# Performance work log

Measured on AMD Instinct MI355X. Metric: run time of the kernel, lower is better.

The kernel has to match this reference:

```python
import jax, jax.numpy as jnp
import numpy as np

ALPHA = 0.2  # LeakyReLU negative slope


def _gat_layer(x, xq, src, dst, W_l, a_l, N):
    # x, xq: [N, Din]; W_l: [Din, D]; a_l: [2*D]
    h = x @ W_l            # [N, D]
    hq = xq @ W_l          # [N, D]
    D = W_l.shape[1]
    # a @ cat(hq[src], h[dst]) splits into two per-node dot products
    sq = hq @ a_l[:D]      # [N]
    sn = h @ a_l[D:]       # [N]
    s = sq[src] + sn[dst]  # [E]
    e = jnp.exp(-jnp.where(s >= 0, s, ALPHA * s))          # [E]
    rowsum = jax.ops.segment_sum(e, src, num_segments=N)    # [N]
    agg = jax.ops.segment_sum(e[:, None] * h[dst], src, num_segments=N)  # [N, D]
    denom = jnp.where(rowsum == 0, 1.0, rowsum)[:, None]
    h_prime = agg / denom
    # torch replaces NaN (0/0) with 0; isolated nodes -> 0
    return jnp.where(rowsum[:, None] == 0, 0.0, h_prime)


def setup_inputs() -> dict:
    key = jax.random.key(0)
    k1, k2, k3, k4, k5 = jax.random.split(key, 5)
    B, N, D, E, L = 2, 20000, 256, 320000, 2
    nodes = jax.random.normal(k1, (B, N, D), dtype=jnp.float32)
    nodes_query = jax.random.normal(k2, (B, N, D), dtype=jnp.float32)
    W = jax.random.normal(k3, (L, D, D), dtype=jnp.float32) * 0.088  # xavier_normal gain=1.414
    a = jax.random.normal(k4, (L, 2 * D), dtype=jnp.float32) * 0.074
    edges = jax.random.randint(k5, (B, 2, E), 0, N, dtype=jnp.int32)
    return {"nodes": nodes, "nodes_query": nodes_query, "W": W, "a": a, "edges": edges}


def reference(nodes, nodes_query, W, a, edges):
    B, N, D = nodes.shape
    L = W.shape[0]

    def per_graph(x, xq, e):
        src, dst = e[0], e[1]
        h = x
        for l in range(L):  # small fixed layer count
            h = _gat_layer(h, xq, src, dst, W[l], a[l], N)
        return h

    out = jax.vmap(per_graph)(nodes, nodes_query, edges)
    return out + nodes  # residual
```

## Files before the change

### kernel.cpp

```cpp
#include <hip/hip_runtime.h>
#include <hip/hip_fp16.h>
#include <math.h>

constexpr int N = 20000, D = 256, E = 320000, B = 2, L = 2;

typedef __bf16 bf16x8 __attribute__((ext_vector_type(8)));
typedef float f32x4 __attribute__((ext_vector_type(4)));

__device__ __forceinline__ unsigned short f2bf(float f) {
  unsigned int u = __float_as_uint(f);
  u = (u + 0x7FFF + ((u >> 16) & 1)) >> 16;
  return (unsigned short)u;
}
__device__ __forceinline__ unsigned short f2h(float f) {
  __half h = __float2half(f);
  return *(unsigned short*)&h;
}
__device__ __forceinline__ float2 h2f(unsigned int u) {
  __half2 hv = *reinterpret_cast<__half2*>(&u);
  return __half22float2(hv);
}

__global__ void tobf_kernel(const float* __restrict__ in, unsigned short* __restrict__ out,
                            int n8) {
  int i = blockIdx.x * blockDim.x + threadIdx.x;
  if (i < n8) {
    float4 v0 = ((const float4*)in)[i * 2];
    float4 v1 = ((const float4*)in)[i * 2 + 1];
    unsigned short t[8] = {f2bf(v0.x), f2bf(v0.y), f2bf(v0.z), f2bf(v0.w),
                           f2bf(v1.x), f2bf(v1.y), f2bf(v1.z), f2bf(v1.w)};
    ((uint4*)out)[i] = *(uint4*)t;
  }
}

__global__ void count_kernel(const int* __restrict__ edges, int* __restrict__ counts) {
  int e = blockIdx.x * blockDim.x + threadIdx.x;
  if (e < B * E) {
    int b = (e >= E) ? 1 : 0;
    int s = edges[(size_t)b * E + e];
    atomicAdd(&counts[b * N + s], 1);
  }
}

__global__ __launch_bounds__(1024) void scan_kernel(const int* __restrict__ counts,
                                                    int* __restrict__ rowstart) {
  constexpr int CHUNK = 20;
  __shared__ int sums[1024];
  int b = blockIdx.x;
  const int* c = counts + b * N;
  int* rs = rowstart + b * (N + 1);
  int tid = threadIdx.x;
  int base = tid * CHUNK;
  int local[CHUNK];
  int s = 0;
#pragma unroll
  for (int i = 0; i < CHUNK; ++i) {
    int g = base + i;
    int v = (g < N) ? c[g] : 0;
    local[i] = s;
    s += v;
  }
  sums[tid] = s;
  __syncthreads();
  for (int off = 1; off < 1024; off <<= 1) {
    int t = (tid >= off) ? sums[tid - off] : 0;
    __syncthreads();
    sums[tid] += t;
    __syncthreads();
  }
  int prev = (tid == 0) ? 0 : sums[tid - 1];
#pragma unroll
  for (int i = 0; i < CHUNK; ++i) {
    int g = base + i;
    if (g < N) rs[g] = prev + local[i];
  }
  if (tid == 1023) rs[N] = sums[1023];
}

__global__ void scatter_kernel(const int* __restrict__ edges, const int* __restrict__ rowstart,
                               int* __restrict__ fill, int* __restrict__ csr) {
  int e = blockIdx.x * blockDim.x + threadIdx.x;
  if (e < B * E) {
    int b = (e >= E) ? 1 : 0;
    int s = edges[(size_t)b * E + e];
    int d = edges[(size_t)(b + 1) * E + e];
    int p = rowstart[b * (N + 1) + s] + atomicAdd(&fill[b * N + s], 1);
    csr[(size_t)b * E + p] = d;
  }
}

__global__ void wt_kernel(const float* __restrict__ W, unsigned short* __restrict__ Wt) {
  __shared__ float t[16][17];
  int l = blockIdx.z;
  int k = blockIdx.y * 16 + threadIdx.y;
  int n = blockIdx.x * 16 + threadIdx.x;
  t[threadIdx.y][threadIdx.x] = W[l * 65536 + k * 256 + n];
  __syncthreads();
  int nn = blockIdx.x * 16 + threadIdx.y;
  int kk = blockIdx.y * 16 + threadIdx.x;
  Wt[l * 65536 + nn * 256 + kk] = f2bf(t[threadIdx.x][threadIdx.y]);
}

__global__ void wa_kernel(const float* __restrict__ W, const float* __restrict__ a,
                          float* __restrict__ wa) {
  int l = blockIdx.x;
  int k = threadIdx.x;
  float s = 0.f;
  for (int d = 0; d < D; ++d) s += W[l * 65536 + k * D + d] * a[l * 2 * D + d];
  wa[l * D + k] = s;
}

__global__ void sq_kernel(const float* __restrict__ xq, const float* __restrict__ wa,
                          float* __restrict__ sq) {
  int wave = (blockIdx.x * blockDim.x + threadIdx.x) >> 6;
  int lane = threadIdx.x & 63;
  int b = blockIdx.y;
  if (wave >= N) return;
  const float4 xv = *(const float4*)(xq + ((size_t)b * N + wave) * D + (lane << 2));
  const float4 w0 = *(const float4*)(wa + (lane << 2));
  const float4 w1 = *(const float4*)(wa + D + (lane << 2));
  float s0 = xv.x * w0.x + xv.y * w0.y + xv.z * w0.z + xv.w * w0.w;
  float s1 = xv.x * w1.x + xv.y * w1.y + xv.z * w1.z + xv.w * w1.w;
  for (int off = 32; off; off >>= 1) {
    s0 += __shfl_down(s0, off);
    s1 += __shfl_down(s1, off);
  }
  if (lane == 0) {
    sq[(b * 2 + 0) * N + wave] = s0;
    sq[(b * 2 + 1) * N + wave] = s1;
  }
}

__global__ __launch_bounds__(256) void gemm_mfma(const unsigned short* __restrict__ A,
                                                 const unsigned short* __restrict__ Wt,
                                                 unsigned short* __restrict__ Ch,
                                                 const float* __restrict__ a2,
                                                 float* __restrict__ sn, int M) {
  __shared__ unsigned short As[128 * 32];
  __shared__ unsigned short Bs[64 * 32];
  int z = blockIdx.z;
  const unsigned short* Az = A + (size_t)z * M * 256;
  unsigned short* Cz = Ch + (size_t)z * M * 256;
  float* snz = sn + (size_t)z * M;
  int tid = threadIdx.x;
  int bm = blockIdx.y * 128, bn = blockIdx.x * 64;
  int wv = tid >> 6, lane = tid & 63;
  int lm = lane & 15, lq = lane >> 4;
  f32x4 acc[2][4] = {};

  for (int k0 = 0; k0 < 256; k0 += 32) {
    int m = tid >> 1, kb = (tid & 1) << 4;
    if (bm + m < M) {
      const unsigned short* ap = Az + (size_t)(bm + m) * 256 + k0 + kb;
      *(uint4*)&As[m * 32 + kb] = *(const uint4*)ap;
      *(uint4*)&As[m * 32 + kb + 8] = *(const uint4*)(ap + 8);
    } else {
      uint4 z4 = make_uint4(0, 0, 0, 0);
      *(uint4*)&As[m * 32 + kb] = z4;
      *(uint4*)&As[m * 32 + kb + 8] = z4;
    }
    int nn = tid >> 2, kb2 = (tid & 3) << 3;
    *(uint4*)&Bs[nn * 32 + kb2] = *(const uint4*)(Wt + (size_t)(bn + nn) * 256 + k0 + kb2);
    __syncthreads();

    bf16x8 af0 = *(const bf16x8*)&As[(wv * 32 + lm) * 32 + lq * 8];
    bf16x8 af1 = *(const bf16x8*)&As[(wv * 32 + 16 + lm) * 32 + lq * 8];
#pragma unroll
    for (int nf = 0; nf < 4; ++nf) {
      bf16x8 bfr = *(const bf16x8*)&Bs[(nf * 16 + lm) * 32 + lq * 8];
      acc[0][nf] = __builtin_amdgcn_mfma_f32_16x16x32_bf16(af0, bfr, acc[0][nf], 0, 0, 0);
      acc[1][nf] = __builtin_amdgcn_mfma_f32_16x16x32_bf16(af1, bfr, acc[1][nf], 0, 0, 0);
    }
    __syncthreads();
  }

  float a2v[4];
#pragma unroll
  for (int nf = 0; nf < 4; ++nf) a2v[nf] = a2[bn + nf * 16 + lm];
#pragma unroll
  for (int f = 0; f < 2; ++f) {
#pragma unroll
    for (int r = 0; r < 4; ++r) {
      int row = bm + wv * 32 + f * 16 + lq * 4 + r;
      if (row < M) {
        float partial = 0.f;
#pragma unroll
        for (int nf = 0; nf < 4; ++nf) {
          float v = acc[f][nf][r];
          Cz[(size_t)row * 256 + bn + nf * 16 + lm] = f2h(v);
          partial += v * a2v[nf];
        }
        partial += __shfl_xor(partial, 1);
        partial += __shfl_xor(partial, 2);
        partial += __shfl_xor(partial, 4);
        partial += __shfl_xor(partial, 8);
        if (lm == 0) atomicAdd(&snz[row], partial);
      }
    }
  }
}

__global__ __launch_bounds__(256) void agg_kernel(const int* __restrict__ rowstart,
                                                  const int* __restrict__ csr,
                                                  const float* __restrict__ sq_all,
                                                  const float* __restrict__ sn,
                                                  const unsigned short* __restrict__ hhf,
                                                  const float* __restrict__ resid,
                                                  float* __restrict__ outf,
                                                  unsigned short* __restrict__ outbf, int l) {
  int b = blockIdx.y;
  int tid = threadIdx.x, wv = tid >> 6, lane = tid & 63;
  int node = blockIdx.x * 4 + wv;
  if (node >= N) return;
  int eg = lane >> 5, dl = lane & 31;
  const int* rs = rowstart + b * (N + 1);
  const int* cs = csr + (size_t)b * E;
  const float* snb = sn + (size_t)b * N;
  const unsigned short* hb = hhf + (size_t)b * N * 256;
  int beg = rs[node], end = rs[node + 1];
  float sqv = sq_all[((b << 1) + l) * N + node];
  float wsum = 0.f;
  float acc[8] = {};
  for (int c0 = beg; c0 < end; c0 += 64) {
    int cnt = min(end - c0, 64);
    int idx = 0;
    float w = 0.f;
    if (lane < cnt) {
      idx = cs[c0 + lane];
      float s = sqv + snb[idx];
      float lr = (s >= 0.f) ? s : 0.2f * s;
      w = __expf(-lr);
    }
    wsum += w;
#pragma unroll 4
    for (int j = eg; j < cnt; j += 2) {
      int dsti = __shfl(idx, j);
      float wj = __shfl(w, j);
      uint4 hv = *(const uint4*)(hb + (size_t)dsti * 256 + (dl << 3));
      float2 f0 = h2f(hv.x), f1 = h2f(hv.y), f2 = h2f(hv.z), f3 = h2f(hv.w);
      acc[0] = fmaf(wj, f0.x, acc[0]);
      acc[1] = fmaf(wj, f0.y, acc[1]);
      acc[2] = fmaf(wj, f1.x, acc[2]);
      acc[3] = fmaf(wj, f1.y, acc[3]);
      acc[4] = fmaf(wj, f2.x, acc[4]);
      acc[5] = fmaf(wj, f2.y, acc[5]);
      acc[6] = fmaf(wj, f3.x, acc[6]);
      acc[7] = fmaf(wj, f3.y, acc[7]);
    }
  }
  for (int off = 32; off; off >>= 1) wsum += __shfl_xor(wsum, off);
#pragma unroll
  for (int i = 0; i < 8; ++i) acc[i] += __shfl_xor(acc[i], 32);
  float inv = (wsum > 0.f) ? 1.f / wsum : 0.f;
  float o0 = (eg ? acc[4] : acc[0]) * inv;
  float o1 = (eg ? acc[5] : acc[1]) * inv;
  float o2 = (eg ? acc[6] : acc[2]) * inv;
  float o3 = (eg ? acc[7] : acc[3]) * inv;
  size_t rowoff = ((size_t)b * N + node) * 256 + (dl << 3) + (eg << 2);
  if (outbf) {
    unsigned short t[4] = {f2bf(o0), f2bf(o1), f2bf(o2), f2bf(o3)};
    *(uint2*)(outbf + rowoff) = *(uint2*)t;
  } else {
    const float4 rv = *(const float4*)(resid + rowoff);
    *(float4*)(outf + rowoff) = make_float4(o0 + rv.x, o1 + rv.y, o2 + rv.z, o3 + rv.w);
  }
}

extern "C" void kernel_launch(void* const* d_in, const int* in_sizes, int n_in,
                              void* d_out, int out_size, void* d_ws, size_t ws_size,
                              hipStream_t stream) {
  const float* nodes = (const float*)d_in[0];
  const float* nodesq = (const float*)d_in[1];
  const float* W = (const float*)d_in[2];
  const float* a = (const float*)d_in[3];
  const int* edges = (const int*)d_in[4];
  float* out = (float*)d_out;

  const size_t ND = (size_t)N * D;
  unsigned short* hhf = (unsigned short*)d_ws;
  unsigned short* h1bf = hhf + (size_t)B * ND;
  unsigned short* nbf = h1bf + (size_t)B * ND;
  unsigned short* Wt = nbf + (size_t)B * ND;
  float* ws_f = (float*)(Wt + (size_t)L * D * D);
  float* sn = ws_f;
  float* sq_all = sn + B * N;
  float* wa = sq_all + (size_t)B * L * N;
  int* wsi = (int*)(wa + L * D);
  int* counts = wsi;
  int* fill = counts + B * N;
  int* rowstart = fill + B * N;
  int* csr = rowstart + B * (N + 1);

  wt_kernel<<<dim3(16, 16, 2), dim3(16, 16), 0, stream>>>(W, Wt);
  wa_kernel<<<2, 256, 0, stream>>>(W, a, wa);
  int n8 = (int)(B * ND / 8);
  tobf_kernel<<<(n8 + 255) / 256, 256, 0, stream>>>(nodes, nbf, n8);

  hipMemsetAsync(counts, 0, (size_t)2 * B * N * sizeof(int), stream);
  count_kernel<<<(B * E + 255) / 256, 256, 0, stream>>>(edges, counts);
  scan_kernel<<<B, 1024, 0, stream>>>(counts, rowstart);
  scatter_kernel<<<(B * E + 255) / 256, 256, 0, stream>>>(edges, rowstart, fill, csr);

  int nwave_blocks = (N * 64 + 255) / 256;
  sq_kernel<<<dim3(nwave_blocks, B), 256, 0, stream>>>(nodesq, wa, sq_all);

  for (int l = 0; l < L; ++l) {
    const float* al2 = a + (size_t)l * 2 * D + D;
    const unsigned short* Acur = (l == 0) ? nbf : h1bf;
    hipMemsetAsync(sn, 0, (size_t)B * N * sizeof(float), stream);
    gemm_mfma<<<dim3(4, (N + 127) / 128, B), 256, 0, stream>>>(Acur, Wt + (size_t)l * D * D,
                                                               hhf, al2, sn, N);
    bool last = (l == L - 1);
    agg_kernel<<<dim3((N + 3) / 4, B), 256, 0, stream>>>(rowstart, csr, sq_all, sn, hhf,
                                                         last ? nodes : nullptr,
                                                         last ? out : nullptr,
                                                         last ? nullptr : h1bf, l);
  }
}
```

Measured before the change: 358.4 us.

## Merge preprocessing launches, drop memsets, and software-pipeline row gathers in aggregation

Several small setup kernels (weight transpose, W·a, bf16 conversion, sq projection, edge counting) and the memsets are merged into two multi-role launches. Zeroing of the sn buffers and the counts/fill arrays is folded into the prep kernel by laying them out contiguously. Each layer now gets its own sn buffer, so the per-layer memset goes away. In the aggregation kernel, neighbour feature loads are issued ahead of the exp/weight computation and double-buffered four at a time, to hide gather latency. The cost is higher register pressure in agg_kernel and more complex branching in the fused kernels.

```diff
diff --git a/kernel.cpp b/kernel.cpp
--- a/kernel.cpp
+++ b/kernel.cpp
@@ -21,21 +21,66 @@
   return __half22float2(hv);
 }
 
-__global__ void tobf_kernel(const float* __restrict__ in, unsigned short* __restrict__ out,
-                            int n8) {
-  int i = blockIdx.x * blockDim.x + threadIdx.x;
-  if (i < n8) {
-    float4 v0 = ((const float4*)in)[i * 2];
-    float4 v1 = ((const float4*)in)[i * 2 + 1];
+__global__ __launch_bounds__(256) void prep_kernel(const float* __restrict__ W,
+                                                   const float* __restrict__ a,
+                                                   unsigned short* __restrict__ Wt,
+                                                   float* __restrict__ wa,
+                                                   uint4* __restrict__ zbase) {
+  int bi = blockIdx.x, tid = threadIdx.x;
+  if (bi < 512) {
+    __shared__ float t[16][17];
+    int l = bi >> 8, rem = bi & 255;
+    int by = rem >> 4, bx = rem & 15;
+    int tx = tid & 15, ty = tid >> 4;
+    t[ty][tx] = W[l * 65536 + (by * 16 + ty) * 256 + bx * 16 + tx];
+    __syncthreads();
+    Wt[l * 65536 + (bx * 16 + ty) * 256 + by * 16 + tx] = f2bf(t[tx][ty]);
+  } else if (bi < 514) {
+    int l = bi - 512;
+    float s = 0.f;
+    for (int d = 0; d < D; ++d) s += W[l * 65536 + tid * D + d] * a[l * 2 * D + d];
+    wa[l * D + tid] = s;
+  } else {
+    int zi = (bi - 514) * 256 + tid;
+    if (zi < 40000) zbase[zi] = make_uint4(0, 0, 0, 0);
+  }
+}
+
+__global__ __launch_bounds__(256) void tsc_kernel(const float* __restrict__ nodes,
+                                                  unsigned short* __restrict__ nbf,
+                                                  const float* __restrict__ xq,
+                                                  const float* __restrict__ wa,
+                                                  float* __restrict__ sq,
+                                                  const int* __restrict__ edges,
+                                                  int* __restrict__ counts) {
+  int bi = blockIdx.x, tid = threadIdx.x;
+  if (bi < 10000) {
+    int b = (bi >= 5000) ? 1 : 0;
+    int blk = bi - b * 5000;
+    int wave = blk * 4 + (tid >> 6);
+    int lane = tid & 63;
+    const float4 xv = *(const float4*)(xq + ((size_t)b * N + wave) * D + (lane << 2));
+    const float4 w0 = *(const float4*)(wa + (lane << 2));
+    const float4 w1 = *(const float4*)(wa + D + (lane << 2));
+    float s0 = xv.x * w0.x + xv.y * w0.y + xv.z * w0.z + xv.w * w0.w;
+    float s1 = xv.x * w1.x + xv.y * w1.y + xv.z * w1.z + xv.w * w1.w;
+    for (int off = 32; off; off >>= 1) {
+      s0 += __shfl_down(s0, off);
+      s1 += __shfl_down(s1, off);
+    }
+    if (lane == 0) {
+      sq[(b * 2 + 0) * N + wave] = s0;
+      sq[(b * 2 + 1) * N + wave] = s1;
+    }
+  } else if (bi < 15000) {
+    int i = (bi - 10000) * 256 + tid;
+    float4 v0 = ((const float4*)nodes)[i * 2];
+    float4 v1 = ((const float4*)nodes)[i * 2 + 1];
     unsigned short t[8] = {f2bf(v0.x), f2bf(v0.y), f2bf(v0.z), f2bf(v0.w),
                            f2bf(v1.x), f2bf(v1.y), f2bf(v1.z), f2bf(v1.w)};
-    ((uint4*)out)[i] = *(uint4*)t;
-  }
-}
-
-__global__ void count_kernel(const int* __restrict__ edges, int* __restrict__ counts) {
-  int e = blockIdx.x * blockDim.x + threadIdx.x;
-  if (e < B * E) {
+    ((uint4*)nbf)[i] = *(uint4*)t;
+  } else {
+    int e = (bi - 15000) * 256 + tid;
     int b = (e >= E) ? 1 : 0;
     int s = edges[(size_t)b * E + e];
     atomicAdd(&counts[b * N + s], 1);
@@ -86,48 +131,6 @@
     int d = edges[(size_t)(b + 1) * E + e];
     int p = rowstart[b * (N + 1) + s] + atomicAdd(&fill[b * N + s], 1);
     csr[(size_t)b * E + p] = d;
-  }
-}
-
-__global__ void wt_kernel(const float* __restrict__ W, unsigned short* __restrict__ Wt) {
-  __shared__ float t[16][17];
-  int l = blockIdx.z;
-  int k = blockIdx.y * 16 + threadIdx.y;
-  int n = blockIdx.x * 16 + threadIdx.x;
-  t[threadIdx.y][threadIdx.x] = W[l * 65536 + k * 256 + n];
-  __syncthreads();
-  int nn = blockIdx.x * 16 + threadIdx.y;
-  int kk = blockIdx.y * 16 + threadIdx.x;
-  Wt[l * 65536 + nn * 256 + kk] = f2bf(t[threadIdx.x][threadIdx.y]);
-}
-
-__global__ void wa_kernel(const float* __restrict__ W, const float* __restrict__ a,
-                          float* __restrict__ wa) {
-  int l = blockIdx.x;
-  int k = threadIdx.x;
-  float s = 0.f;
-  for (int d = 0; d < D; ++d) s += W[l * 65536 + k * D + d] * a[l * 2 * D + d];
-  wa[l * D + k] = s;
-}
-
-__global__ void sq_kernel(const float* __restrict__ xq, const float* __restrict__ wa,
-                          float* __restrict__ sq) {
-  int wave = (blockIdx.x * blockDim.x + threadIdx.x) >> 6;
-  int lane = threadIdx.x & 63;
-  int b = blockIdx.y;
-  if (wave >= N) return;
-  const float4 xv = *(const float4*)(xq + ((size_t)b * N + wave) * D + (lane << 2));
-  const float4 w0 = *(const float4*)(wa + (lane << 2));
-  const float4 w1 = *(const float4*)(wa + D + (lane << 2));
-  float s0 = xv.x * w0.x + xv.y * w0.y + xv.z * w0.z + xv.w * w0.w;
-  float s1 = xv.x * w1.x + xv.y * w1.y + xv.z * w1.z + xv.w * w1.w;
-  for (int off = 32; off; off >>= 1) {
-    s0 += __shfl_down(s0, off);
-    s1 += __shfl_down(s1, off);
-  }
-  if (lane == 0) {
-    sq[(b * 2 + 0) * N + wave] = s0;
-    sq[(b * 2 + 1) * N + wave] = s1;
   }
 }
 
@@ -224,28 +227,50 @@
   for (int c0 = beg; c0 < end; c0 += 64) {
     int cnt = min(end - c0, 64);
     int idx = 0;
-    float w = 0.f;
+    float snv = 0.f;
     if (lane < cnt) {
       idx = cs[c0 + lane];
-      float s = sqv + snb[idx];
-      float lr = (s >= 0.f) ? s : 0.2f * s;
-      w = __expf(-lr);
-    }
+      snv = snb[idx];
+    }
+    int nj = (cnt - eg + 1) >> 1;
+    uint4 hv[4];
+#pragma unroll
+    for (int u = 0; u < 4; ++u) {
+      int dsti = __shfl(idx, eg + 2 * u);
+      if (u < nj) hv[u] = *(const uint4*)(hb + (size_t)dsti * 256 + (dl << 3));
+    }
+    float s = sqv + snv;
+    float lr = (s >= 0.f) ? s : 0.2f * s;
+    float w = (lane < cnt) ? __expf(-lr) : 0.f;
     wsum += w;
-#pragma unroll 4
-    for (int j = eg; j < cnt; j += 2) {
-      int dsti = __shfl(idx, j);
-      float wj = __shfl(w, j);
-      uint4 hv = *(const uint4*)(hb + (size_t)dsti * 256 + (dl << 3));
-      float2 f0 = h2f(hv.x), f1 = h2f(hv.y), f2 = h2f(hv.z), f3 = h2f(hv.w);
-      acc[0] = fmaf(wj, f0.x, acc[0]);
-      acc[1] = fmaf(wj, f0.y, acc[1]);
-      acc[2] = fmaf(wj, f1.x, acc[2]);
-      acc[3] = fmaf(wj, f1.y, acc[3]);
-      acc[4] = fmaf(wj, f2.x, acc[4]);
-      acc[5] = fmaf(wj, f2.y, acc[5]);
-      acc[6] = fmaf(wj, f3.x, acc[6]);
-      acc[7] = fmaf(wj, f3.y, acc[7]);
+    for (int u0 = 0; u0 < nj; u0 += 4) {
+      uint4 hn[4];
+#pragma unroll
+      for (int u = 0; u < 4; ++u) {
+        int uu = u0 + 4 + u;
+        int js = eg + 2 * uu;
+        js = (js < 63) ? js : 63;
+        int dsti = __shfl(idx, js);
+        if (uu < nj) hn[u] = *(const uint4*)(hb + (size_t)dsti * 256 + (dl << 3));
+      }
+#pragma unroll
+      for (int u = 0; u < 4; ++u) {
+        int uu = u0 + u;
+        if (uu < nj) {
+          float wj = __shfl(w, eg + 2 * uu);
+          float2 f0 = h2f(hv[u].x), f1 = h2f(hv[u].y), f2 = h2f(hv[u].z), f3 = h2f(hv[u].w);
+          acc[0] = fmaf(wj, f0.x, acc[0]);
+          acc[1] = fmaf(wj, f0.y, acc[1]);
+          acc[2] = fmaf(wj, f1.x, acc[2]);
+          acc[3] = fmaf(wj, f1.y, acc[3]);
+          acc[4] = fmaf(wj, f2.x, acc[4]);
+          acc[5] = fmaf(wj, f2.y, acc[5]);
+          acc[6] = fmaf(wj, f3.x, acc[6]);
+          acc[7] = fmaf(wj, f3.y, acc[7]);
+        }
+      }
+#pragma unroll
+      for (int u = 0; u < 4; ++u) hv[u] = hn[u];
     }
   }
   for (int off = 32; off; off >>= 1) wsum += __shfl_xor(wsum, off);
@@ -281,37 +306,28 @@
   unsigned short* h1bf = hhf + (size_t)B * ND;
   unsigned short* nbf = h1bf + (size_t)B * ND;
   unsigned short* Wt = nbf + (size_t)B * ND;
-  float* ws_f = (float*)(Wt + (size_t)L * D * D);
-  float* sn = ws_f;
-  float* sq_all = sn + B * N;
+  float* sn0 = (float*)(Wt + (size_t)L * D * D);
+  float* sn1 = sn0 + B * N;
+  int* counts = (int*)(sn1 + B * N);
+  int* fill = counts + B * N;
+  float* sq_all = (float*)(fill + B * N);
   float* wa = sq_all + (size_t)B * L * N;
-  int* wsi = (int*)(wa + L * D);
-  int* counts = wsi;
-  int* fill = counts + B * N;
-  int* rowstart = fill + B * N;
+  int* rowstart = (int*)(wa + L * D);
   int* csr = rowstart + B * (N + 1);
 
-  wt_kernel<<<dim3(16, 16, 2), dim3(16, 16), 0, stream>>>(W, Wt);
-  wa_kernel<<<2, 256, 0, stream>>>(W, a, wa);
-  int n8 = (int)(B * ND / 8);
-  tobf_kernel<<<(n8 + 255) / 256, 256, 0, stream>>>(nodes, nbf, n8);
-
-  hipMemsetAsync(counts, 0, (size_t)2 * B * N * sizeof(int), stream);
-  count_kernel<<<(B * E + 255) / 256, 256, 0, stream>>>(edges, counts);
+  prep_kernel<<<671, 256, 0, stream>>>(W, a, Wt, wa, (uint4*)sn0);
+  tsc_kernel<<<17500, 256, 0, stream>>>(nodes, nbf, nodesq, wa, sq_all, edges, counts);
   scan_kernel<<<B, 1024, 0, stream>>>(counts, rowstart);
   scatter_kernel<<<(B * E + 255) / 256, 256, 0, stream>>>(edges, rowstart, fill, csr);
-
-  int nwave_blocks = (N * 64 + 255) / 256;
-  sq_kernel<<<dim3(nwave_blocks, B), 256, 0, stream>>>(nodesq, wa, sq_all);
 
   for (int l = 0; l < L; ++l) {
     const float* al2 = a + (size_t)l * 2 * D + D;
     const unsigned short* Acur = (l == 0) ? nbf : h1bf;
-    hipMemsetAsync(sn, 0, (size_t)B * N * sizeof(float), stream);
+    float* snl = (l == 0) ? sn0 : sn1;
     gemm_mfma<<<dim3(4, (N + 127) / 128, B), 256, 0, stream>>>(Acur, Wt + (size_t)l * D * D,
-                                                               hhf, al2, sn, N);
+                                                               hhf, al2, snl, N);
     bool last = (l == L - 1);
-    agg_kernel<<<dim3((N + 3) / 4, B), 256, 0, stream>>>(rowstart, csr, sq_all, sn, hhf,
+    agg_kernel<<<dim3((N + 3) / 4, B), 256, 0, stream>>>(rowstart, csr, sq_all, snl, hhf,
                                                          last ? nodes : nullptr,
                                                          last ? out : nullptr,
                                                          last ? nullptr : h1bf, l);
```

After: 335.6 us. 1.07x faster.
